# Kernel optimization log

Measured on AMD Instinct MI355X. Metric: run time of the kernel, lower is better.

Reference implementation:

```python
import jax, jax.numpy as jnp
import numpy as np

NU = 500000   # num_users
NI = 500000   # num_items
E = 128       # embedding_dim
F = 172       # feature_dim
B = 65536     # number of events in the batch
MSG = 2 * E + F  # GRU input dim = 428


def _gru_cell(x, h, wih, whh, bih, bhh):
    # PyTorch GRUCell: gates ordered (r, z, n)
    gi = x @ wih.T + bih            # [B, 3E]
    gh = h @ whh.T + bhh            # [B, 3E]
    ir, iz, in_ = jnp.split(gi, 3, axis=-1)
    hr, hz, hn = jnp.split(gh, 3, axis=-1)
    r = jax.nn.sigmoid(ir + hr)
    z = jax.nn.sigmoid(iz + hz)
    n = jnp.tanh(in_ + r * hn)
    return (1.0 - z) * n + z * h


def setup_inputs() -> dict:
    key = jax.random.key(0)
    ks = jax.random.split(key, 18)
    s = 0.05  # init scale ~ 1/sqrt(E)
    return {
        "user_ids": jax.random.randint(ks[0], (B,), 0, NU),
        "item_ids": jax.random.randint(ks[1], (B,), 0, NI),
        "timestamps": jax.random.uniform(ks[2], (B,), dtype=jnp.float32) * 1000.0,
        "features": jax.random.normal(ks[3], (B, F), dtype=jnp.float32),
        "query_time": 1200,
        "memory": jax.random.normal(ks[4], (NU + NI, E), dtype=jnp.float32) * 0.1,
        "last_time": jax.random.uniform(ks[5], (NU + NI,), dtype=jnp.float32) * 1000.0,
        "time_w": jax.random.normal(ks[6], (E,), dtype=jnp.float32) * 0.01,  # Linear(1,E,bias=False)
        "u_wih": jax.random.normal(ks[7], (3 * E, MSG), dtype=jnp.float32) * s,
        "u_whh": jax.random.normal(ks[8], (3 * E, E), dtype=jnp.float32) * s,
        "u_bih": jax.random.normal(ks[9], (3 * E,), dtype=jnp.float32) * s,
        "u_bhh": jax.random.normal(ks[10], (3 * E,), dtype=jnp.float32) * s,
        "i_wih": jax.random.normal(ks[11], (3 * E, MSG), dtype=jnp.float32) * s,
        "i_whh": jax.random.normal(ks[12], (3 * E, E), dtype=jnp.float32) * s,
        "i_bih": jax.random.normal(ks[13], (3 * E,), dtype=jnp.float32) * s,
        "i_bhh": jax.random.normal(ks[14], (3 * E,), dtype=jnp.float32) * s,
        "gate_w": jax.random.normal(ks[15], (E, 2 * E), dtype=jnp.float32) * s,
        "gate_b": jnp.zeros((E,), dtype=jnp.float32),
        "pred_w": jax.random.normal(ks[16], (E, E), dtype=jnp.float32) * s,
        "pred_b": jnp.zeros((E,), dtype=jnp.float32),
    }


def reference(user_ids, item_ids, timestamps, features, query_time, memory, last_time,
              time_w, u_wih, u_whh, u_bih, u_bhh, i_wih, i_whh, i_bih, i_bhh,
              gate_w, gate_b, pred_w, pred_b):
    item_nodes = item_ids + NU  # offset items into global node id space
    # per-event gather from node memory
    old_user = memory[user_ids]          # [B, E]
    old_item = memory[item_nodes]        # [B, E]
    last_u = last_time[user_ids]         # [B]
    last_i = last_time[item_nodes]       # [B]

    du = (timestamps - last_u)[:, None]  # [B, 1]
    di = (timestamps - last_i)[:, None]
    # time projection: emb * (1 + Linear(dt))
    proj_user = old_user * (1.0 + du * time_w)
    proj_item = old_item * (1.0 + di * time_w)

    d_query = (jnp.float32(query_time) - last_u)[:, None]
    query_user = old_user * (1.0 + d_query * time_w)

    # peer message mode: user_msg = proj_item, item_msg = proj_user
    user_input = jnp.concatenate([proj_user, proj_item, features], axis=-1)  # [B, MSG]
    item_input = jnp.concatenate([proj_item, proj_user, features], axis=-1)

    new_user = _gru_cell(user_input, old_user, u_wih, u_whh, u_bih, u_bhh)
    new_item = _gru_cell(item_input, old_item, i_wih, i_whh, i_bih, i_bhh)

    # memory gate: g*new + (1-g)*old
    gu = jax.nn.sigmoid(jnp.concatenate([old_user, new_user], axis=-1) @ gate_w.T + gate_b)
    gi = jax.nn.sigmoid(jnp.concatenate([old_item, new_item], axis=-1) @ gate_w.T + gate_b)
    new_user = gu * new_user + (1.0 - gu) * old_user
    new_item = gi * new_item + (1.0 - gi) * old_item

    pred_item_emb = query_user @ pred_w.T + pred_b
    return (pred_item_emb, new_user, new_item)
```

## Files before the change

kernel.cpp:

```cpp
#include <hip/hip_runtime.h>
#include <hip/hip_bf16.h>
#include <cstdint>
#include <cstddef>

#define CNU 500000
#define CB  65536
#define CE  128
#define CF  172
#define EV  64

typedef unsigned short ushort_t;
typedef __attribute__((ext_vector_type(8))) short b8;
typedef __attribute__((ext_vector_type(4))) short b4;
typedef __attribute__((ext_vector_type(4))) float f4;
typedef __attribute__((ext_vector_type(4))) float f32x4;

#define MFMA16(a,b,c) __builtin_amdgcn_mfma_f32_16x16x32_bf16((a),(b),(c),0,0,0)

#define NTL4(p)   __builtin_nontemporal_load((const f32x4*)(p))
#define NTLI(p)   __builtin_nontemporal_load(p)
#define NTS(v, p) __builtin_nontemporal_store((v), (p))

#define FRAG 512
#define U_KT 18
#define U_NT 24
#define U_SZ (U_NT*U_KT*FRAG)
#define PU_OFF 0
#define PI_OFF U_SZ
#define PG_OFF (2*U_SZ)
#define G_SZ (8*8*FRAG)
#define PP_OFF (PG_OFF + G_SZ)
#define P_SZ (8*4*FRAG)

#define SWZ(r, c) ((c) ^ (((r) & 7) << 3))
#define AFRAG(T, r, c) (*(const b8*)&(T)[(r)][SWZ((r), (c))])

__device__ __forceinline__ unsigned pk2bf(float a, float b) {
  __hip_bfloat162 h = __float22bfloat162_rn(make_float2(a, b));
  return *reinterpret_cast<unsigned*>(&h);
}
__device__ __forceinline__ ushort_t f2bf(float f) {
  unsigned u = __float_as_uint(f);
  return (ushort_t)((u + 0x7FFFu + ((u >> 16) & 1u)) >> 16);
}
__device__ __forceinline__ float bf2f(ushort_t h) {
  return __uint_as_float(((unsigned)h) << 16);
}
__device__ __forceinline__ float sigmoid_(float x) { return 1.0f/(1.0f+__expf(-x)); }
__device__ __forceinline__ float tanh_(float x) { float e=__expf(2.0f*x); return 1.0f-2.0f/(e+1.0f); }

struct __align__(16) SLds {
  ushort_t PU[EV][128];
  ushort_t PI[EV][128];
  ushort_t FE[EV][192];
  ushort_t OU[EV][128];
  ushort_t OI[EV][128];
  ushort_t QU[EV][128];
};

extern "C" __global__ void prep_weights(
    const float* __restrict__ u_wih, const float* __restrict__ u_whh,
    const float* __restrict__ i_wih, const float* __restrict__ i_whh,
    const float* __restrict__ gate_w, const float* __restrict__ pred_w,
    ushort_t* __restrict__ ws)
{
  const int stride = gridDim.x * blockDim.x;
  const int tid = blockIdx.x * blockDim.x + threadIdx.x;
  for (int i = tid; i < U_SZ; i += stride) {
    const int nt = i / (U_KT*FRAG);
    const int r1 = i - nt*(U_KT*FRAG);
    const int kt = r1 / FRAG;
    const int e  = r1 - kt*FRAG;
    const int l  = e >> 3, j = e & 7;
    const int n  = nt*16 + (l & 15);
    const int k  = (l >> 4)*8 + j;
    float vu, vi;
    if (kt < 14) {
      const int kk = kt*32 + k;
      vu = (kk < 428) ? u_wih[(size_t)n*428 + kk] : 0.0f;
      vi = (kk < 428) ? i_wih[(size_t)n*428 + kk] : 0.0f;
    } else {
      const int kk = (kt - 14)*32 + k;
      vu = u_whh[(size_t)n*128 + kk];
      vi = i_whh[(size_t)n*128 + kk];
    }
    ws[PU_OFF + i] = f2bf(vu);
    ws[PI_OFF + i] = f2bf(vi);
  }
  for (int i = tid; i < G_SZ; i += stride) {
    const int nt = i / (8*FRAG);
    const int r1 = i - nt*(8*FRAG);
    const int kt = r1 / FRAG;
    const int e  = r1 - kt*FRAG;
    const int l  = e >> 3, j = e & 7;
    const int n  = nt*16 + (l & 15);
    const int kk = kt*32 + (l >> 4)*8 + j;
    ws[PG_OFF + i] = f2bf(gate_w[(size_t)n*256 + kk]);
  }
  for (int i = tid; i < P_SZ; i += stride) {
    const int nt = i / (4*FRAG);
    const int r1 = i - nt*(4*FRAG);
    const int kt = r1 / FRAG;
    const int e  = r1 - kt*FRAG;
    const int l  = e >> 3, j = e & 7;
    const int n  = nt*16 + (l & 15);
    const int kk = kt*32 + (l >> 4)*8 + j;
    ws[PP_OFF + i] = f2bf(pred_w[(size_t)n*128 + kk]);
  }
}

extern "C" __global__ void __launch_bounds__(512, 2)
jodie_main(const int* __restrict__ user_ids, const int* __restrict__ item_ids,
           const float* __restrict__ timestamps, const float* __restrict__ features,
           const int* __restrict__ query_time, const float* __restrict__ memv,
           const float* __restrict__ last_time, const float* __restrict__ time_w,
           const float* __restrict__ u_bih, const float* __restrict__ u_bhh,
           const float* __restrict__ i_bih, const float* __restrict__ i_bhh,
           const float* __restrict__ gate_b, const float* __restrict__ pred_b,
           const ushort_t* __restrict__ ws, float* __restrict__ d_out)
{
  __shared__ SLds s;
  const int t  = threadIdx.x;
  const int e0 = blockIdx.x * EV;

  {
    const int c8 = (t & 15) * 8;
    const float qt = (float)query_time[0];
    const float4 tw0 = *(const float4*)&time_w[c8];
    const float4 tw1 = *(const float4*)&time_w[c8 + 4];
    const float twv[8] = {tw0.x,tw0.y,tw0.z,tw0.w, tw1.x,tw1.y,tw1.z,tw1.w};
#pragma unroll
    for (int ep = 0; ep < 2; ++ep) {
      const int e  = ep*32 + (t >> 4);
      const int ge = e0 + e;
      const int u   = NTLI(&user_ids[ge]);
      const int itn = NTLI(&item_ids[ge]) + CNU;
      const float ts = NTLI(&timestamps[ge]);
      const float lu = NTLI(&last_time[u]);
      const float li = NTLI(&last_time[itn]);
      const float du = ts - lu, di = ts - li, dq = qt - lu;

      const f32x4 ou0 = NTL4(&memv[(size_t)u  *CE + c8]);
      const f32x4 ou1 = NTL4(&memv[(size_t)u  *CE + c8 + 4]);
      const f32x4 oi0 = NTL4(&memv[(size_t)itn*CE + c8]);
      const f32x4 oi1 = NTL4(&memv[(size_t)itn*CE + c8 + 4]);
      const float ouv[8] = {ou0[0],ou0[1],ou0[2],ou0[3], ou1[0],ou1[1],ou1[2],ou1[3]};
      const float oiv[8] = {oi0[0],oi0[1],oi0[2],oi0[3], oi1[0],oi1[1],oi1[2],oi1[3]};

      union U8 { unsigned q[4]; b8 v; };
      U8 xu, xi, hu, hi, qv;
#pragma unroll
      for (int j = 0; j < 8; j += 2) {
        xu.q[j>>1] = pk2bf(ouv[j]*(1.0f + du*twv[j]), ouv[j+1]*(1.0f + du*twv[j+1]));
        xi.q[j>>1] = pk2bf(oiv[j]*(1.0f + di*twv[j]), oiv[j+1]*(1.0f + di*twv[j+1]));
        hu.q[j>>1] = pk2bf(ouv[j], ouv[j+1]);
        hi.q[j>>1] = pk2bf(oiv[j], oiv[j+1]);
        qv.q[j>>1] = pk2bf(ouv[j]*(1.0f + dq*twv[j]), ouv[j+1]*(1.0f + dq*twv[j+1]));
      }
      *(b8*)&s.PU[e][SWZ(e, c8)] = xu.v;
      *(b8*)&s.PI[e][SWZ(e, c8)] = xi.v;
      *(b8*)&s.OU[e][SWZ(e, c8)] = hu.v;
      *(b8*)&s.OI[e][SWZ(e, c8)] = hi.v;
      *(b8*)&s.QU[e][SWZ(e, c8)] = qv.v;
    }
  }
  for (int i = t; i < EV*43; i += 512) {
    const int e = i / 43, q = i - e*43;
    const f32x4 fv = NTL4(&features[(size_t)(e0 + e)*CF + q*4]);
    union { unsigned q2[2]; b4 v; } fb;
    fb.q2[0] = pk2bf(fv[0], fv[1]);
    fb.q2[1] = pk2bf(fv[2], fv[3]);
    *(b4*)&s.FE[e][SWZ(e, q*4)] = fb.v;
  }
  for (int i = t; i < EV*20; i += 512) {
    const int e = i / 20, c = 172 + (i - e*20);
    s.FE[e][SWZ(e, c)] = 0;
  }
  __syncthreads();

  const int wv   = t >> 6, l = t & 63;
  const int lrow = l & 15;
  const int lk   = (l >> 4) * 8;
  const int col  = wv*16 + lrow;

  {
    const float bp = pred_b[col];
    f4 ap[4];
#pragma unroll
    for (int m = 0; m < 4; ++m) ap[m] = (f4){bp,bp,bp,bp};
    const ushort_t* WP = ws + PP_OFF + (size_t)wv*4*FRAG + l*8;
#pragma unroll
    for (int kt = 0; kt < 4; ++kt) {
      b8 fp = *(const b8*)(WP + (size_t)kt*FRAG);
#pragma unroll
      for (int m = 0; m < 4; ++m) {
        b8 a = AFRAG(s.QU, m*16 + lrow, 32*kt + lk);
        ap[m] = MFMA16(a, fp, ap[m]);
      }
    }
#pragma unroll
    for (int m = 0; m < 4; ++m)
#pragma unroll
      for (int r4 = 0; r4 < 4; ++r4) {
        const int row = m*16 + (l >> 4)*4 + r4;
        NTS(ap[m][r4], &d_out[(size_t)(e0 + row)*CE + col]);
      }
  }
  __syncthreads();

  const float bru = u_bih[col]     + u_bhh[col];
  const float bzu = u_bih[col+128] + u_bhh[col+128];
  const float bnu = u_bih[col+256];
  const float bhu = u_bhh[col+256];
  const float bri = i_bih[col]     + i_bhh[col];
  const float bzi = i_bih[col+128] + i_bhh[col+128];
  const float bni = i_bih[col+256];
  const float bhi = i_bhh[col+256];

  f4 aru[4], azu[4], anu[4], ari[4], azi[4], ani[4];
#pragma unroll
  for (int m = 0; m < 4; ++m) {
    aru[m] = (f4){bru,bru,bru,bru};  azu[m] = (f4){bzu,bzu,bzu,bzu};
    anu[m] = (f4){bnu,bnu,bnu,bnu};  ari[m] = (f4){bri,bri,bri,bri};
    azi[m] = (f4){bzi,bzi,bzi,bzi};  ani[m] = (f4){bni,bni,bni,bni};
  }

  const ushort_t* Wru = ws + PU_OFF + (size_t)(wv     )*U_KT*FRAG + l*8;
  const ushort_t* Wzu = ws + PU_OFF + (size_t)(wv +  8)*U_KT*FRAG + l*8;
  const ushort_t* Wnu = ws + PU_OFF + (size_t)(wv + 16)*U_KT*FRAG + l*8;
  const ushort_t* Wri = ws + PI_OFF + (size_t)(wv     )*U_KT*FRAG + l*8;
  const ushort_t* Wzi = ws + PI_OFF + (size_t)(wv +  8)*U_KT*FRAG + l*8;
  const ushort_t* Wni = ws + PI_OFF + (size_t)(wv + 16)*U_KT*FRAG + l*8;

#define GI_STEP(TILE, pf, ktu, kti)                                          \
  {                                                                          \
    b8 a_[4];                                                                \
    _Pragma("unroll")                                                        \
    for (int m = 0; m < 4; ++m) a_[m] = AFRAG(TILE, m*16 + lrow, 32*(pf) + lk); \
    b8 fru = *(const b8*)(Wru + (size_t)(ktu)*FRAG);                         \
    b8 fzu = *(const b8*)(Wzu + (size_t)(ktu)*FRAG);                         \
    b8 fnu = *(const b8*)(Wnu + (size_t)(ktu)*FRAG);                         \
    b8 fri = *(const b8*)(Wri + (size_t)(kti)*FRAG);                         \
    b8 fzi = *(const b8*)(Wzi + (size_t)(kti)*FRAG);                         \
    b8 fni = *(const b8*)(Wni + (size_t)(kti)*FRAG);                         \
    _Pragma("unroll")                                                        \
    for (int m = 0; m < 4; ++m) {                                            \
      aru[m] = MFMA16(a_[m], fru, aru[m]);                                   \
      azu[m] = MFMA16(a_[m], fzu, azu[m]);                                   \
      anu[m] = MFMA16(a_[m], fnu, anu[m]);                                   \
      ari[m] = MFMA16(a_[m], fri, ari[m]);                                   \
      azi[m] = MFMA16(a_[m], fzi, azi[m]);                                   \
      ani[m] = MFMA16(a_[m], fni, ani[m]);                                   \
    }                                                                        \
  }

#pragma unroll
  for (int pf = 0; pf < 4; ++pf) GI_STEP(s.PU, pf, pf, pf + 4)
#pragma unroll
  for (int pf = 0; pf < 4; ++pf) GI_STEP(s.PI, pf, pf + 4, pf)
#pragma unroll
  for (int pf = 0; pf < 6; ++pf) GI_STEP(s.FE, pf, pf + 8, pf + 8)
#undef GI_STEP

  {
    f4 ah[4];
#pragma unroll
    for (int m = 0; m < 4; ++m) ah[m] = (f4){bhu,bhu,bhu,bhu};
#pragma unroll
    for (int kt = 0; kt < 4; ++kt) {
      b8 fr = *(const b8*)(Wru + (size_t)(14+kt)*FRAG);
      b8 fz = *(const b8*)(Wzu + (size_t)(14+kt)*FRAG);
      b8 fn = *(const b8*)(Wnu + (size_t)(14+kt)*FRAG);
#pragma unroll
      for (int m = 0; m < 4; ++m) {
        b8 h = AFRAG(s.OU, m*16 + lrow, 32*kt + lk);
        aru[m] = MFMA16(h, fr, aru[m]);
        azu[m] = MFMA16(h, fz, azu[m]);
        ah[m]  = MFMA16(h, fn, ah[m]);
      }
    }
#pragma unroll
    for (int m = 0; m < 4; ++m)
#pragma unroll
      for (int r4 = 0; r4 < 4; ++r4) {
        const int row = m*16 + (l >> 4)*4 + r4;
        const float rr = sigmoid_(aru[m][r4]);
        const float zz = sigmoid_(azu[m][r4]);
        const float nn = tanh_(anu[m][r4] + rr*ah[m][r4]);
        const float h  = bf2f(s.OU[row][SWZ(row, col)]);
        s.QU[row][SWZ(row, col)] = f2bf((1.0f - zz)*nn + zz*h);
      }
  }
  __syncthreads();

  {
    f4 ah[4];
#pragma unroll
    for (int m = 0; m < 4; ++m) ah[m] = (f4){bhi,bhi,bhi,bhi};
#pragma unroll
    for (int kt = 0; kt < 4; ++kt) {
      b8 fr = *(const b8*)(Wri + (size_t)(14+kt)*FRAG);
      b8 fz = *(const b8*)(Wzi + (size_t)(14+kt)*FRAG);
      b8 fn = *(const b8*)(Wni + (size_t)(14+kt)*FRAG);
#pragma unroll
      for (int m = 0; m < 4; ++m) {
        b8 h = AFRAG(s.OI, m*16 + lrow, 32*kt + lk);
        ari[m] = MFMA16(h, fr, ari[m]);
        azi[m] = MFMA16(h, fz, azi[m]);
        ah[m]  = MFMA16(h, fn, ah[m]);
      }
    }
#pragma unroll
    for (int m = 0; m < 4; ++m)
#pragma unroll
      for (int r4 = 0; r4 < 4; ++r4) {
        const int row = m*16 + (l >> 4)*4 + r4;
        const float rr = sigmoid_(ari[m][r4]);
        const float zz = sigmoid_(azi[m][r4]);
        const float nn = tanh_(ani[m][r4] + rr*ah[m][r4]);
        const float h  = bf2f(s.OI[row][SWZ(row, col)]);
        s.PU[row][SWZ(row, col)] = f2bf((1.0f - zz)*nn + zz*h);
      }
  }
  __syncthreads();

  {
    const float gb = gate_b[col];
    f4 agu[4], agi[4];
#pragma unroll
    for (int m = 0; m < 4; ++m) { agu[m] = (f4){gb,gb,gb,gb}; agi[m] = agu[m]; }
    const ushort_t* WG = ws + PG_OFF + (size_t)wv*8*FRAG + l*8;
#pragma unroll
    for (int kt = 0; kt < 8; ++kt) {
      b8 fg = *(const b8*)(WG + (size_t)kt*FRAG);
#pragma unroll
      for (int m = 0; m < 4; ++m) {
        b8 au = (kt < 4) ? AFRAG(s.OU, m*16 + lrow, 32*kt + lk)
                         : AFRAG(s.QU, m*16 + lrow, 32*(kt-4) + lk);
        b8 ai = (kt < 4) ? AFRAG(s.OI, m*16 + lrow, 32*kt + lk)
                         : AFRAG(s.PU, m*16 + lrow, 32*(kt-4) + lk);
        agu[m] = MFMA16(au, fg, agu[m]);
        agi[m] = MFMA16(ai, fg, agi[m]);
      }
    }
    float* __restrict__ outu = d_out + (size_t)CB*CE;
    float* __restrict__ outi = d_out + (size_t)2*CB*CE;
#pragma unroll
    for (int m = 0; m < 4; ++m)
#pragma unroll
      for (int r4 = 0; r4 < 4; ++r4) {
        const int row = m*16 + (l >> 4)*4 + r4;
        const float gu = sigmoid_(agu[m][r4]);
        const float gi = sigmoid_(agi[m][r4]);
        const float hu  = bf2f(s.OU[row][SWZ(row, col)]);
        const float hpu = bf2f(s.QU[row][SWZ(row, col)]);
        const float hi  = bf2f(s.OI[row][SWZ(row, col)]);
        const float hpi = bf2f(s.PU[row][SWZ(row, col)]);
        NTS(gu*hpu + (1.0f - gu)*hu, &outu[(size_t)(e0 + row)*CE + col]);
        NTS(gi*hpi + (1.0f - gi)*hi, &outi[(size_t)(e0 + row)*CE + col]);
      }
  }
}

extern "C" void kernel_launch(void* const* d_in, const int* in_sizes, int n_in,
                              void* d_out, int out_size, void* d_ws, size_t ws_size,
                              hipStream_t stream) {
  const int*   user_ids   = (const int*)d_in[0];
  const int*   item_ids   = (const int*)d_in[1];
  const float* timestamps = (const float*)d_in[2];
  const float* features   = (const float*)d_in[3];
  const int*   query_time = (const int*)d_in[4];
  const float* memv       = (const float*)d_in[5];
  const float* last_time  = (const float*)d_in[6];
  const float* time_w     = (const float*)d_in[7];
  const float* u_wih = (const float*)d_in[8];
  const float* u_whh = (const float*)d_in[9];
  const float* u_bih = (const float*)d_in[10];
  const float* u_bhh = (const float*)d_in[11];
  const float* i_wih = (const float*)d_in[12];
  const float* i_whh = (const float*)d_in[13];
  const float* i_bih = (const float*)d_in[14];
  const float* i_bhh = (const float*)d_in[15];
  const float* gate_w = (const float*)d_in[16];
  const float* gate_b = (const float*)d_in[17];
  const float* pred_w = (const float*)d_in[18];
  const float* pred_b = (const float*)d_in[19];
  ushort_t* ws = (ushort_t*)d_ws;
  float* out = (float*)d_out;

  prep_weights<<<dim3(256), dim3(256), 0, stream>>>(u_wih, u_whh, i_wih, i_whh,
                                                    gate_w, pred_w, ws);
  jodie_main<<<dim3(CB/EV), dim3(512), 0, stream>>>(user_ids, item_ids, timestamps,
                                                    features, query_time, memv,
                                                    last_time, time_w,
                                                    u_bih, u_bhh, i_bih, i_bhh,
                                                    gate_b, pred_b, ws, out);
}
```

Measured before the change: 142.9 us.

## Split gather into separate staging kernel writing MFMA-fragment layout into output buffer

Adds a stage_gather kernel that does the random memory/last_time gathers, time projection and feature bf16 conversion. It writes the results in MFMA A-fragment order into the output buffer, which serves as scratch. The main kernel then bulk-copies a contiguous 32KB-per-block tile into LDS, computes the query projection on the fly from OU and a DQ vector, and drops two barriers. The aim is to separate latency-bound gathers from the MFMA compute and raise gather occupancy, at the cost of an extra kernel launch and a round trip through global memory. The main kernel overwrites the scratch region in the output while reading it, which relies on each block touching only its own region.

```diff
diff --git a/kernel.cpp b/kernel.cpp
--- a/kernel.cpp
+++ b/kernel.cpp
@@ -8,10 +8,10 @@
 #define CE  128
 #define CF  172
 #define EV  64
+#define SECB ((size_t)CB*CE*4)
 
 typedef unsigned short ushort_t;
 typedef __attribute__((ext_vector_type(8))) short b8;
-typedef __attribute__((ext_vector_type(4))) short b4;
 typedef __attribute__((ext_vector_type(4))) float f4;
 typedef __attribute__((ext_vector_type(4))) float f32x4;
 
@@ -34,6 +34,7 @@
 
 #define SWZ(r, c) ((c) ^ (((r) & 7) << 3))
 #define AFRAG(T, r, c) (*(const b8*)&(T)[(r)][SWZ((r), (c))])
+#define FR(T, kt, m) (*(const b8*)&(T)[(((kt)*4 + (m))*512) + l*8])
 
 __device__ __forceinline__ unsigned pk2bf(float a, float b) {
   __hip_bfloat162 h = __float22bfloat162_rn(make_float2(a, b));
@@ -49,14 +50,25 @@
 __device__ __forceinline__ float sigmoid_(float x) { return 1.0f/(1.0f+__expf(-x)); }
 __device__ __forceinline__ float tanh_(float x) { float e=__expf(2.0f*x); return 1.0f-2.0f/(e+1.0f); }
 
-struct __align__(16) SLds {
-  ushort_t PU[EV][128];
-  ushort_t PI[EV][128];
-  ushort_t FE[EV][192];
-  ushort_t OU[EV][128];
-  ushort_t OI[EV][128];
-  ushort_t QU[EV][128];
-};
+__device__ __forceinline__ b8 scale8(b8 x, float d, f32x4 t0, f32x4 t1) {
+  union { ushort_t u[8]; unsigned q[4]; b8 v; } in, out;
+  in.v = x;
+  const float tt[8] = {t0[0],t0[1],t0[2],t0[3], t1[0],t1[1],t1[2],t1[3]};
+#pragma unroll
+  for (int j = 0; j < 4; ++j) {
+    float a = bf2f(in.u[2*j]);
+    float b = bf2f(in.u[2*j+1]);
+    a = fmaf(a, d*tt[2*j],   a);
+    b = fmaf(b, d*tt[2*j+1], b);
+    out.q[j] = pk2bf(a, b);
+  }
+  return out.v;
+}
+
+__device__ __forceinline__ float frag_elem(const ushort_t* T, int row, int col) {
+  const int kt = col >> 5, q = (col & 31) >> 3, j = col & 7;
+  return bf2f(T[(size_t)((kt*4 + (row >> 4))*512 + ((row & 15) + 16*q)*8 + j)]);
+}
 
 extern "C" __global__ void prep_weights(
     const float* __restrict__ u_wih, const float* __restrict__ u_whh,
@@ -109,73 +121,128 @@
   }
 }
 
+extern "C" __global__ void __launch_bounds__(512, 4)
+stage_gather(const int* __restrict__ user_ids, const int* __restrict__ item_ids,
+             const float* __restrict__ timestamps, const float* __restrict__ features,
+             const int* __restrict__ query_time, const float* __restrict__ memv,
+             const float* __restrict__ last_time, const float* __restrict__ time_w,
+             char* __restrict__ outb)
+{
+  const int t  = threadIdx.x;
+  const int e0 = blockIdx.x * 32;
+  {
+    const int c8 = (t & 15) * 8;
+    const int e  = t >> 4;
+    const int ge = e0 + e;
+    const int bb = ge >> 6, e64 = ge & 63;
+    const int mt = e64 >> 4, row = e64 & 15;
+    const int kt = c8 >> 5, q = (c8 & 31) >> 3;
+    const size_t fo = (size_t)(((kt*4 + mt)*512 + (row + 16*q)*8) * 2);
+
+    const int u   = NTLI(&user_ids[ge]);
+    const int itn = NTLI(&item_ids[ge]) + CNU;
+    const float ts = NTLI(&timestamps[ge]);
+    const float lu = last_time[u];
+    const float li = last_time[itn];
+    const float qt = (float)query_time[0];
+    const float du = ts - lu, di = ts - li;
+
+    const float4 tw0 = *(const float4*)&time_w[c8];
+    const float4 tw1 = *(const float4*)&time_w[c8 + 4];
+    const float twv[8] = {tw0.x,tw0.y,tw0.z,tw0.w, tw1.x,tw1.y,tw1.z,tw1.w};
+    const f32x4 ou0 = NTL4(&memv[(size_t)u  *CE + c8]);
+    const f32x4 ou1 = NTL4(&memv[(size_t)u  *CE + c8 + 4]);
+    const f32x4 oi0 = NTL4(&memv[(size_t)itn*CE + c8]);
+    const f32x4 oi1 = NTL4(&memv[(size_t)itn*CE + c8 + 4]);
+    const float ouv[8] = {ou0[0],ou0[1],ou0[2],ou0[3], ou1[0],ou1[1],ou1[2],ou1[3]};
+    const float oiv[8] = {oi0[0],oi0[1],oi0[2],oi0[3], oi1[0],oi1[1],oi1[2],oi1[3]};
+
+    union U8 { unsigned q_[4]; b8 v; };
+    U8 xu, xi, hu, hi;
+#pragma unroll
+    for (int j = 0; j < 8; j += 2) {
+      xu.q_[j>>1] = pk2bf(ouv[j]*(1.0f + du*twv[j]), ouv[j+1]*(1.0f + du*twv[j+1]));
+      xi.q_[j>>1] = pk2bf(oiv[j]*(1.0f + di*twv[j]), oiv[j+1]*(1.0f + di*twv[j+1]));
+      hu.q_[j>>1] = pk2bf(ouv[j], ouv[j+1]);
+      hi.q_[j>>1] = pk2bf(oiv[j], oiv[j+1]);
+    }
+    char* W0 = outb + (size_t)bb*32768;
+    char* W1 = outb + SECB + (size_t)bb*32768;
+    *(b8*)(W0 + fo)         = xu.v;
+    *(b8*)(W0 + 16384 + fo) = xi.v;
+    *(b8*)(W1 + fo)         = hu.v;
+    *(b8*)(W1 + 16384 + fo) = hi.v;
+    if ((t & 15) == 0)
+      *(float*)(outb + 2*SECB + (size_t)bb*32768 + 24576 + (size_t)e64*4) = qt - lu;
+  }
+  for (int i = t; i < 32*24; i += 512) {
+    const int e = i / 24, c = i - e*24;
+    const int fkt = c >> 2, fq = c & 3;
+    const int ge = e0 + e;
+    const int bb = ge >> 6, e64 = ge & 63;
+    const int mt = e64 >> 4, row = e64 & 15;
+    const int col0 = fkt*32 + fq*8;
+    float v[8];
+    if (col0 + 8 <= CF) {
+      const f32x4 x0 = NTL4(&features[(size_t)ge*CF + col0]);
+      const f32x4 x1 = NTL4(&features[(size_t)ge*CF + col0 + 4]);
+      v[0]=x0[0]; v[1]=x0[1]; v[2]=x0[2]; v[3]=x0[3];
+      v[4]=x1[0]; v[5]=x1[1]; v[6]=x1[2]; v[7]=x1[3];
+    } else {
+#pragma unroll
+      for (int j = 0; j < 8; ++j) {
+        const int cc = col0 + j;
+        v[j] = (cc < CF) ? features[(size_t)ge*CF + cc] : 0.0f;
+      }
+    }
+    union { unsigned q_[4]; b8 v8; } fb;
+    fb.q_[0] = pk2bf(v[0], v[1]);  fb.q_[1] = pk2bf(v[2], v[3]);
+    fb.q_[2] = pk2bf(v[4], v[5]);  fb.q_[3] = pk2bf(v[6], v[7]);
+    *(b8*)(outb + 2*SECB + (size_t)bb*32768
+           + (size_t)(((fkt*4 + mt)*512 + (row + 16*fq)*8) * 2)) = fb.v8;
+  }
+}
+
+struct __align__(16) SLdsB {
+  ushort_t PU[8192];
+  ushort_t PI[8192];
+  ushort_t OU[8192];
+  ushort_t OI[8192];
+  ushort_t FE[12288];
+  float    DQ[64];
+  char     pad2[32768 - 24576 - 256];
+  ushort_t HU[EV][128];
+  ushort_t HI[EV][128];
+  float    TW[128];
+};
+
 extern "C" __global__ void __launch_bounds__(512, 2)
-jodie_main(const int* __restrict__ user_ids, const int* __restrict__ item_ids,
-           const float* __restrict__ timestamps, const float* __restrict__ features,
-           const int* __restrict__ query_time, const float* __restrict__ memv,
-           const float* __restrict__ last_time, const float* __restrict__ time_w,
+jodie_main(const float* __restrict__ time_w,
            const float* __restrict__ u_bih, const float* __restrict__ u_bhh,
            const float* __restrict__ i_bih, const float* __restrict__ i_bhh,
            const float* __restrict__ gate_b, const float* __restrict__ pred_b,
            const ushort_t* __restrict__ ws, float* __restrict__ d_out)
 {
-  __shared__ SLds s;
+  __shared__ SLdsB s;
   const int t  = threadIdx.x;
   const int e0 = blockIdx.x * EV;
-
-  {
-    const int c8 = (t & 15) * 8;
-    const float qt = (float)query_time[0];
-    const float4 tw0 = *(const float4*)&time_w[c8];
-    const float4 tw1 = *(const float4*)&time_w[c8 + 4];
-    const float twv[8] = {tw0.x,tw0.y,tw0.z,tw0.w, tw1.x,tw1.y,tw1.z,tw1.w};
-#pragma unroll
-    for (int ep = 0; ep < 2; ++ep) {
-      const int e  = ep*32 + (t >> 4);
-      const int ge = e0 + e;
-      const int u   = NTLI(&user_ids[ge]);
-      const int itn = NTLI(&item_ids[ge]) + CNU;
-      const float ts = NTLI(&timestamps[ge]);
-      const float lu = NTLI(&last_time[u]);
-      const float li = NTLI(&last_time[itn]);
-      const float du = ts - lu, di = ts - li, dq = qt - lu;
-
-      const f32x4 ou0 = NTL4(&memv[(size_t)u  *CE + c8]);
-      const f32x4 ou1 = NTL4(&memv[(size_t)u  *CE + c8 + 4]);
-      const f32x4 oi0 = NTL4(&memv[(size_t)itn*CE + c8]);
-      const f32x4 oi1 = NTL4(&memv[(size_t)itn*CE + c8 + 4]);
-      const float ouv[8] = {ou0[0],ou0[1],ou0[2],ou0[3], ou1[0],ou1[1],ou1[2],ou1[3]};
-      const float oiv[8] = {oi0[0],oi0[1],oi0[2],oi0[3], oi1[0],oi1[1],oi1[2],oi1[3]};
-
-      union U8 { unsigned q[4]; b8 v; };
-      U8 xu, xi, hu, hi, qv;
-#pragma unroll
-      for (int j = 0; j < 8; j += 2) {
-        xu.q[j>>1] = pk2bf(ouv[j]*(1.0f + du*twv[j]), ouv[j+1]*(1.0f + du*twv[j+1]));
-        xi.q[j>>1] = pk2bf(oiv[j]*(1.0f + di*twv[j]), oiv[j+1]*(1.0f + di*twv[j+1]));
-        hu.q[j>>1] = pk2bf(ouv[j], ouv[j+1]);
-        hi.q[j>>1] = pk2bf(oiv[j], oiv[j+1]);
-        qv.q[j>>1] = pk2bf(ouv[j]*(1.0f + dq*twv[j]), ouv[j+1]*(1.0f + dq*twv[j+1]));
-      }
-      *(b8*)&s.PU[e][SWZ(e, c8)] = xu.v;
-      *(b8*)&s.PI[e][SWZ(e, c8)] = xi.v;
-      *(b8*)&s.OU[e][SWZ(e, c8)] = hu.v;
-      *(b8*)&s.OI[e][SWZ(e, c8)] = hi.v;
-      *(b8*)&s.QU[e][SWZ(e, c8)] = qv.v;
-    }
-  }
-  for (int i = t; i < EV*43; i += 512) {
-    const int e = i / 43, q = i - e*43;
-    const f32x4 fv = NTL4(&features[(size_t)(e0 + e)*CF + q*4]);
-    union { unsigned q2[2]; b4 v; } fb;
-    fb.q2[0] = pk2bf(fv[0], fv[1]);
-    fb.q2[1] = pk2bf(fv[2], fv[3]);
-    *(b4*)&s.FE[e][SWZ(e, q*4)] = fb.v;
-  }
-  for (int i = t; i < EV*20; i += 512) {
-    const int e = i / 20, c = 172 + (i - e*20);
-    s.FE[e][SWZ(e, c)] = 0;
-  }
+  char* outb = (char*)d_out;
+
+  {
+    const char* W0 = outb + (size_t)blockIdx.x*32768;
+    const char* W1 = outb + SECB + (size_t)blockIdx.x*32768;
+    const char* W2 = outb + 2*SECB + (size_t)blockIdx.x*32768;
+    char* lb = (char*)&s;
+#pragma unroll
+    for (int k = 0; k < 12; ++k) {
+      const int idx = k*512 + t;
+      const char* src = (idx < 2048) ? (W0 + (size_t)idx*16)
+                      : (idx < 4096) ? (W1 + (size_t)(idx - 2048)*16)
+                                     : (W2 + (size_t)(idx - 4096)*16);
+      *(b8*)(lb + (size_t)idx*16) = *(const b8*)src;
+    }
+  }
+  if (t < 32) *(float4*)&s.TW[t*4] = *(const float4*)&time_w[t*4];
   __syncthreads();
 
   const int wv   = t >> 6, l = t & 63;
@@ -183,18 +250,27 @@
   const int lk   = (l >> 4) * 8;
   const int col  = wv*16 + lrow;
 
+  const ushort_t* Wru = ws + PU_OFF + (size_t)(wv     )*U_KT*FRAG + l*8;
+  const ushort_t* Wzu = ws + PU_OFF + (size_t)(wv +  8)*U_KT*FRAG + l*8;
+  const ushort_t* Wnu = ws + PU_OFF + (size_t)(wv + 16)*U_KT*FRAG + l*8;
+  const ushort_t* Wri = ws + PI_OFF + (size_t)(wv     )*U_KT*FRAG + l*8;
+  const ushort_t* Wzi = ws + PI_OFF + (size_t)(wv +  8)*U_KT*FRAG + l*8;
+  const ushort_t* Wni = ws + PI_OFF + (size_t)(wv + 16)*U_KT*FRAG + l*8;
+
   {
     const float bp = pred_b[col];
+    const ushort_t* WP = ws + PP_OFF + (size_t)wv*4*FRAG + l*8;
     f4 ap[4];
 #pragma unroll
     for (int m = 0; m < 4; ++m) ap[m] = (f4){bp,bp,bp,bp};
-    const ushort_t* WP = ws + PP_OFF + (size_t)wv*4*FRAG + l*8;
 #pragma unroll
     for (int kt = 0; kt < 4; ++kt) {
       b8 fp = *(const b8*)(WP + (size_t)kt*FRAG);
+      const f32x4 t0 = *(const f32x4*)&s.TW[32*kt + lk];
+      const f32x4 t1 = *(const f32x4*)&s.TW[32*kt + lk + 4];
 #pragma unroll
       for (int m = 0; m < 4; ++m) {
-        b8 a = AFRAG(s.QU, m*16 + lrow, 32*kt + lk);
+        b8 a = scale8(FR(s.OU, kt, m), s.DQ[m*16 + lrow], t0, t1);
         ap[m] = MFMA16(a, fp, ap[m]);
       }
     }
@@ -206,7 +282,6 @@
         NTS(ap[m][r4], &d_out[(size_t)(e0 + row)*CE + col]);
       }
   }
-  __syncthreads();
 
   const float bru = u_bih[col]     + u_bhh[col];
   const float bzu = u_bih[col+128] + u_bhh[col+128];
@@ -225,18 +300,11 @@
     azi[m] = (f4){bzi,bzi,bzi,bzi};  ani[m] = (f4){bni,bni,bni,bni};
   }
 
-  const ushort_t* Wru = ws + PU_OFF + (size_t)(wv     )*U_KT*FRAG + l*8;
-  const ushort_t* Wzu = ws + PU_OFF + (size_t)(wv +  8)*U_KT*FRAG + l*8;
-  const ushort_t* Wnu = ws + PU_OFF + (size_t)(wv + 16)*U_KT*FRAG + l*8;
-  const ushort_t* Wri = ws + PI_OFF + (size_t)(wv     )*U_KT*FRAG + l*8;
-  const ushort_t* Wzi = ws + PI_OFF + (size_t)(wv +  8)*U_KT*FRAG + l*8;
-  const ushort_t* Wni = ws + PI_OFF + (size_t)(wv + 16)*U_KT*FRAG + l*8;
-
 #define GI_STEP(TILE, pf, ktu, kti)                                          \
   {                                                                          \
     b8 a_[4];                                                                \
     _Pragma("unroll")                                                        \
-    for (int m = 0; m < 4; ++m) a_[m] = AFRAG(TILE, m*16 + lrow, 32*(pf) + lk); \
+    for (int m = 0; m < 4; ++m) a_[m] = FR(TILE, pf, m);                     \
     b8 fru = *(const b8*)(Wru + (size_t)(ktu)*FRAG);                         \
     b8 fzu = *(const b8*)(Wzu + (size_t)(ktu)*FRAG);                         \
     b8 fnu = *(const b8*)(Wnu + (size_t)(ktu)*FRAG);                         \
@@ -273,7 +341,7 @@
       b8 fn = *(const b8*)(Wnu + (size_t)(14+kt)*FRAG);
 #pragma unroll
       for (int m = 0; m < 4; ++m) {
-        b8 h = AFRAG(s.OU, m*16 + lrow, 32*kt + lk);
+        b8 h = FR(s.OU, kt, m);
         aru[m] = MFMA16(h, fr, aru[m]);
         azu[m] = MFMA16(h, fz, azu[m]);
         ah[m]  = MFMA16(h, fn, ah[m]);
@@ -287,11 +355,10 @@
         const float rr = sigmoid_(aru[m][r4]);
         const float zz = sigmoid_(azu[m][r4]);
         const float nn = tanh_(anu[m][r4] + rr*ah[m][r4]);
-        const float h  = bf2f(s.OU[row][SWZ(row, col)]);
-        s.QU[row][SWZ(row, col)] = f2bf((1.0f - zz)*nn + zz*h);
-      }
-  }
-  __syncthreads();
+        const float h  = frag_elem(s.OU, row, col);
+        s.HU[row][SWZ(row, col)] = f2bf((1.0f - zz)*nn + zz*h);
+      }
+  }
 
   {
     f4 ah[4];
@@ -304,7 +371,7 @@
       b8 fn = *(const b8*)(Wni + (size_t)(14+kt)*FRAG);
 #pragma unroll
       for (int m = 0; m < 4; ++m) {
-        b8 h = AFRAG(s.OI, m*16 + lrow, 32*kt + lk);
+        b8 h = FR(s.OI, kt, m);
         ari[m] = MFMA16(h, fr, ari[m]);
         azi[m] = MFMA16(h, fz, azi[m]);
         ah[m]  = MFMA16(h, fn, ah[m]);
@@ -318,27 +385,27 @@
         const float rr = sigmoid_(ari[m][r4]);
         const float zz = sigmoid_(azi[m][r4]);
         const float nn = tanh_(ani[m][r4] + rr*ah[m][r4]);
-        const float h  = bf2f(s.OI[row][SWZ(row, col)]);
-        s.PU[row][SWZ(row, col)] = f2bf((1.0f - zz)*nn + zz*h);
+        const float h  = frag_elem(s.OI, row, col);
+        s.HI[row][SWZ(row, col)] = f2bf((1.0f - zz)*nn + zz*h);
       }
   }
   __syncthreads();
 
   {
     const float gb = gate_b[col];
+    const ushort_t* WG = ws + PG_OFF + (size_t)wv*8*FRAG + l*8;
     f4 agu[4], agi[4];
 #pragma unroll
     for (int m = 0; m < 4; ++m) { agu[m] = (f4){gb,gb,gb,gb}; agi[m] = agu[m]; }
-    const ushort_t* WG = ws + PG_OFF + (size_t)wv*8*FRAG + l*8;
 #pragma unroll
     for (int kt = 0; kt < 8; ++kt) {
       b8 fg = *(const b8*)(WG + (size_t)kt*FRAG);
 #pragma unroll
       for (int m = 0; m < 4; ++m) {
-        b8 au = (kt < 4) ? AFRAG(s.OU, m*16 + lrow, 32*kt + lk)
-                         : AFRAG(s.QU, m*16 + lrow, 32*(kt-4) + lk);
-        b8 ai = (kt < 4) ? AFRAG(s.OI, m*16 + lrow, 32*kt + lk)
-                         : AFRAG(s.PU, m*16 + lrow, 32*(kt-4) + lk);
+        b8 au = (kt < 4) ? FR(s.OU, kt, m)
+                         : AFRAG(s.HU, m*16 + lrow, 32*(kt-4) + lk);
+        b8 ai = (kt < 4) ? FR(s.OI, kt, m)
+                         : AFRAG(s.HI, m*16 + lrow, 32*(kt-4) + lk);
         agu[m] = MFMA16(au, fg, agu[m]);
         agi[m] = MFMA16(ai, fg, agi[m]);
       }
@@ -352,10 +419,10 @@
         const int row = m*16 + (l >> 4)*4 + r4;
         const float gu = sigmoid_(agu[m][r4]);
         const float gi = sigmoid_(agi[m][r4]);
-        const float hu  = bf2f(s.OU[row][SWZ(row, col)]);
-        const float hpu = bf2f(s.QU[row][SWZ(row, col)]);
-        const float hi  = bf2f(s.OI[row][SWZ(row, col)]);
-        const float hpi = bf2f(s.PU[row][SWZ(row, col)]);
+        const float hu  = frag_elem(s.OU, row, col);
+        const float hpu = bf2f(s.HU[row][SWZ(row, col)]);
+        const float hi  = frag_elem(s.OI, row, col);
+        const float hpi = bf2f(s.HI[row][SWZ(row, col)]);
         NTS(gu*hpu + (1.0f - gu)*hu, &outu[(size_t)(e0 + row)*CE + col]);
         NTS(gi*hpi + (1.0f - gi)*hi, &outi[(size_t)(e0 + row)*CE + col]);
       }
@@ -390,9 +457,10 @@
 
   prep_weights<<<dim3(256), dim3(256), 0, stream>>>(u_wih, u_whh, i_wih, i_whh,
                                                     gate_w, pred_w, ws);
-  jodie_main<<<dim3(CB/EV), dim3(512), 0, stream>>>(user_ids, item_ids, timestamps,
-                                                    features, query_time, memv,
-                                                    last_time, time_w,
+  stage_gather<<<dim3(CB/32), dim3(512), 0, stream>>>(user_ids, item_ids, timestamps,
+                                                      features, query_time, memv,
+                                                      last_time, time_w, (char*)out);
+  jodie_main<<<dim3(CB/EV), dim3(512), 0, stream>>>(time_w,
                                                     u_bih, u_bhh, i_bih, i_bhh,
                                                     gate_b, pred_b, ws, out);
 }
```

Measured after the change: 164.5 us. 15.2% more time.
